# Optimization experiments

Hardware: AMD Instinct MI355X
Metric: run time of the kernel (lower is better)

The kernel has to match this reference:

```python
import jax, jax.numpy as jnp
import numpy as np

D = 4096  # domain size of every variable X, Y, Z, W


def setup_inputs() -> dict:
    key = jax.random.key(0)
    ks = jax.random.split(key, 7)
    theta0 = jax.random.normal(ks[0], (D, D), dtype=jnp.float32)  # clique (X, Y)
    theta1 = jax.random.normal(ks[1], (D, D), dtype=jnp.float32)  # clique (Y, Z)
    theta2 = jax.random.normal(ks[2], (D, D), dtype=jnp.float32)  # clique (Z, W)
    ops = {f"op{i}": jax.random.randint(ks[3 + i], (2, D), 0, D, dtype=jnp.int32)
           for i in range(4)}
    return {"theta0": theta0, "theta1": theta1, "theta2": theta2, **ops}


def _remap(proc, op, dom):
    # torch: zeros(dom).index_add_(0, op[1], proc[op[0]])
    return jnp.zeros((dom,), proc.dtype).at[op[1]].add(proc[op[0]])


def reference(theta0, theta1, theta2, op0, op1, op2, op3):
    dom = theta0.shape[0]
    # m0: clique0 -> clique1 (forward): sum over X (dim 0), remap Y, broadcast over Z
    m0 = _remap(jnp.sum(theta0, axis=0), op0, dom)
    theta1 = theta1 + m0[:, None]          # reshape_dims [True, False]
    # m1: clique1 -> clique2 (forward): sum over Y (dim 0), remap Z
    m1 = _remap(jnp.sum(theta1, axis=0), op1, dom)
    theta2 = theta2 + m1[:, None]
    # m2: clique2 -> clique1 (backward): sum over W (dim 1), subtract stored fwd msg m1
    m2 = _remap(jnp.sum(theta2, axis=1) - m1, op2, dom)
    theta1 = theta1 + m2[None, :]          # reshape_dims [False, True]
    # m3: clique1 -> clique0 (backward): sum over Z (dim 1), subtract stored fwd msg m0
    m3 = _remap(jnp.sum(theta1, axis=1) - m0, op3, dom)
    theta0 = theta0 + m3[None, :]
    return (theta0, theta1, theta2)
```

## Files before the change

kernel.cpp:

```cpp
#include <hip/hip_runtime.h>

#define D 4096

typedef float fx4 __attribute__((ext_vector_type(4)));


__global__ void __launch_bounds__(256) reduce_all_kernel(
        const float* __restrict__ t0, const float* __restrict__ t1,
        const float* __restrict__ t2, float* __restrict__ ws) {
    int b = blockIdx.x;
    if (b < 512) {
        const float* A = (b < 256) ? t0 : t1;
        float* out = ws + ((b < 256) ? 0 : D);
        int lb = b & 255;
        int c4 = (lb & 3) * 256 + threadIdx.x;
        int r0 = (lb >> 2) * 64;
        const fx4* A4 = (const fx4*)A;
        fx4 s = (fx4){0.f, 0.f, 0.f, 0.f};
        #pragma unroll 8
        for (int r = 0; r < 64; ++r) {
            s += A4[(size_t)(r0 + r) * (D / 4) + c4];
        }
        atomicAdd(&out[c4 * 4 + 0], s.x);
        atomicAdd(&out[c4 * 4 + 1], s.y);
        atomicAdd(&out[c4 * 4 + 2], s.z);
        atomicAdd(&out[c4 * 4 + 3], s.w);
    } else {
        int lb = (b - 512) & 1023;
        const float* A = (b < 1536) ? t1 : t2;
        float* out = ws + ((b < 1536) ? 2 * D : 3 * D);
        int wid = threadIdx.x >> 6, lane = threadIdx.x & 63;
        int row = lb * 4 + wid;
        const fx4* A4 = (const fx4*)(A + (size_t)row * D);
        float s = 0.f;
        #pragma unroll 4
        for (int i = lane; i < D / 4; i += 64) {
            fx4 v = A4[i];
            s += (v.x + v.y) + (v.z + v.w);
        }
        #pragma unroll
        for (int o = 32; o > 0; o >>= 1) s += __shfl_down(s, o);
        if (lane == 0) out[row] = s;
    }
}


__device__ __forceinline__ float block_sum_1024(float v, float* red) {
    #pragma unroll
    for (int o = 32; o > 0; o >>= 1) v += __shfl_down(v, o);
    int lane = threadIdx.x & 63, wid = threadIdx.x >> 6;
    if (lane == 0) red[wid] = v;
    __syncthreads();
    if (threadIdx.x == 0) {
        float t = 0.f;
        #pragma unroll
        for (int w = 0; w < 16; ++w) t += red[w];
        red[0] = t;
    }
    __syncthreads();
    float r = red[0];
    __syncthreads();
    return r;
}

__global__ void __launch_bounds__(1024) messages_kernel(
        const float* __restrict__ ws,
        const int* __restrict__ op0, const int* __restrict__ op1,
        const int* __restrict__ op2, const int* __restrict__ op3,
        float* __restrict__ ws_w) {
    const float* colsum0 = ws;
    const float* colsum1 = ws + D;
    const float* rowsum1 = ws + 2 * D;
    const float* rowsum2 = ws + 3 * D;

    __shared__ float m0[D], m1[D], m2[D], m3[D];
    __shared__ float red[16];
    int tid = threadIdx.x;

    int s0[4], d0[4], s1[4], d1[4], s2[4], d2[4], s3[4], d3[4];
    #pragma unroll
    for (int k = 0; k < 4; ++k) {
        int i = tid + k * 1024;
        s0[k] = op0[i]; d0[k] = op0[D + i];
        s1[k] = op1[i]; d1[k] = op1[D + i];
        s2[k] = op2[i]; d2[k] = op2[D + i];
        s3[k] = op3[i]; d3[k] = op3[D + i];
    }
    float g0[4], g1[4], g2[4], g3[4];
    #pragma unroll
    for (int k = 0; k < 4; ++k) {
        g0[k] = colsum0[s0[k]];
        g1[k] = colsum1[s1[k]];
        g2[k] = rowsum2[s2[k]];
        g3[k] = rowsum1[s3[k]];
    }

    #pragma unroll
    for (int k = 0; k < 4; ++k) {
        int i = tid + k * 1024;
        m0[i] = 0.f; m1[i] = 0.f; m2[i] = 0.f; m3[i] = 0.f;
    }
    __syncthreads();

    #pragma unroll
    for (int k = 0; k < 4; ++k) atomicAdd(&m0[d0[k]], g0[k]);
    __syncthreads();

    float p = 0.f;
    #pragma unroll
    for (int k = 0; k < 4; ++k) p += m0[tid + k * 1024];
    float S0 = block_sum_1024(p, red);

    #pragma unroll
    for (int k = 0; k < 4; ++k) atomicAdd(&m1[d1[k]], g1[k] + S0);
    __syncthreads();

    #pragma unroll
    for (int k = 0; k < 4; ++k)
        atomicAdd(&m2[d2[k]], g2[k] + 4095.0f * m1[s2[k]]);
    __syncthreads();

    p = 0.f;
    #pragma unroll
    for (int k = 0; k < 4; ++k) p += m2[tid + k * 1024];
    float S2 = block_sum_1024(p, red);

    #pragma unroll
    for (int k = 0; k < 4; ++k)
        atomicAdd(&m3[d3[k]], g3[k] + 4095.0f * m0[s3[k]] + S2);
    __syncthreads();

    #pragma unroll
    for (int k = 0; k < 4; ++k) {
        int i = tid + k * 1024;
        ws_w[4 * D + i] = m0[i];
        ws_w[5 * D + i] = m1[i];
        ws_w[6 * D + i] = m2[i];
        ws_w[7 * D + i] = m3[i];
    }
}

__global__ void __launch_bounds__(256) apply_kernel(
        const float* __restrict__ t0, const float* __restrict__ t1,
        const float* __restrict__ t2, const float* __restrict__ msgs,
        float* __restrict__ out) {
    int b = blockIdx.x;
    int mat = b >> 12;
    int row = b & (D - 1);
    const float* m0 = msgs + 0 * D;
    const float* m1 = msgs + 1 * D;
    const float* m2 = msgs + 2 * D;
    const float* m3 = msgs + 3 * D;
    size_t base = (size_t)row * D;
    fx4* dst = (fx4*)(out + (size_t)mat * D * D + base);

    if (mat == 0) {
        const fx4* src = (const fx4*)(t0 + base);
        const fx4* c4 = (const fx4*)m3;
        for (int i = threadIdx.x; i < D / 4; i += 256) {
            fx4 r = src[i] + c4[i];
            __builtin_nontemporal_store(r, &dst[i]);
        }
    } else if (mat == 1) {
        const fx4* src = (const fx4*)(t1 + base);
        const fx4* c4 = (const fx4*)m2;
        float rr = m0[row];
        for (int i = threadIdx.x; i < D / 4; i += 256) {
            fx4 r = src[i] + c4[i] + rr;
            __builtin_nontemporal_store(r, &dst[i]);
        }
    } else {
        const fx4* src = (const fx4*)(t2 + base);
        float rr = m1[row];
        for (int i = threadIdx.x; i < D / 4; i += 256) {
            fx4 r = src[i] + rr;
            __builtin_nontemporal_store(r, &dst[i]);
        }
    }
}

extern "C" void kernel_launch(void* const* d_in, const int* in_sizes, int n_in,
                              void* d_out, int out_size, void* d_ws, size_t ws_size,
                              hipStream_t stream) {
    const float* t0 = (const float*)d_in[0];
    const float* t1 = (const float*)d_in[1];
    const float* t2 = (const float*)d_in[2];
    const int* op0 = (const int*)d_in[3];
    const int* op1 = (const int*)d_in[4];
    const int* op2 = (const int*)d_in[5];
    const int* op3 = (const int*)d_in[6];
    float* out = (float*)d_out;
    float* ws = (float*)d_ws;

    hipMemsetAsync(ws, 0, 2 * D * sizeof(float), stream);

    reduce_all_kernel<<<2560, 256, 0, stream>>>(t0, t1, t2, ws);
    messages_kernel<<<1, 1024, 0, stream>>>(ws, op0, op1, op2, op3, ws);
    apply_kernel<<<3 * D, 256, 0, stream>>>(t0, t1, t2, ws + 4 * D, out);
}
```

Before: 143.8 us.

## Fuse theta1 row/column sums into one pass and drop atomics and memset

```diff
diff --git a/kernel.cpp b/kernel.cpp
--- a/kernel.cpp
+++ b/kernel.cpp
@@ -4,43 +4,79 @@
 
 typedef float fx4 __attribute__((ext_vector_type(4)));
 
+#define P0  0
+#define P1  262144
+#define RS1 524288
+#define RS2 528384
+#define MSG 532480
 
 __global__ void __launch_bounds__(256) reduce_all_kernel(
         const float* __restrict__ t0, const float* __restrict__ t1,
         const float* __restrict__ t2, float* __restrict__ ws) {
     int b = blockIdx.x;
-    if (b < 512) {
-        const float* A = (b < 256) ? t0 : t1;
-        float* out = ws + ((b < 256) ? 0 : D);
-        int lb = b & 255;
-        int c4 = (lb & 3) * 256 + threadIdx.x;
-        int r0 = (lb >> 2) * 64;
-        const fx4* A4 = (const fx4*)A;
-        fx4 s = (fx4){0.f, 0.f, 0.f, 0.f};
+    if (b < 256) {
+        int q = b & 3, s = b >> 2;
+        int c4 = q * 256 + threadIdx.x;
+        int r0 = s * 64;
+        const fx4* A4 = (const fx4*)t0;
+        fx4 acc = (fx4){0.f, 0.f, 0.f, 0.f};
         #pragma unroll 8
-        for (int r = 0; r < 64; ++r) {
-            s += A4[(size_t)(r0 + r) * (D / 4) + c4];
-        }
-        atomicAdd(&out[c4 * 4 + 0], s.x);
-        atomicAdd(&out[c4 * 4 + 1], s.y);
-        atomicAdd(&out[c4 * 4 + 2], s.z);
-        atomicAdd(&out[c4 * 4 + 3], s.w);
+        for (int r = 0; r < 64; ++r)
+            acc += A4[(size_t)(r0 + r) * (D / 4) + c4];
+        ((fx4*)(ws + P0))[(size_t)s * (D / 4) + c4] = acc;
+    } else if (b < 320) {
+        int s = b - 256;
+        int r0 = s * 64;
+        int wid = threadIdx.x >> 6, lane = threadIdx.x & 63;
+        const fx4* A4 = (const fx4*)t1;
+        fx4 acc[16];
+        #pragma unroll
+        for (int j = 0; j < 16; ++j) acc[j] = (fx4){0.f, 0.f, 0.f, 0.f};
+        for (int it = 0; it < 16; ++it) {
+            int row = r0 + it * 4 + wid;
+            const fx4* R = A4 + (size_t)row * (D / 4);
+            float rs = 0.f;
+            #pragma unroll
+            for (int j = 0; j < 16; ++j) {
+                fx4 v = R[lane + 64 * j];
+                acc[j] += v;
+                rs += (v.x + v.y) + (v.z + v.w);
+            }
+            #pragma unroll
+            for (int o = 32; o > 0; o >>= 1) rs += __shfl_down(rs, o);
+            if (lane == 0) ws[RS1 + row] = rs;
+        }
+        __shared__ fx4 cs[D / 4];
+        for (int ww = 0; ww < 4; ++ww) {
+            if (wid == ww) {
+                #pragma unroll
+                for (int j = 0; j < 16; ++j) {
+                    int c = lane + 64 * j;
+                    if (ww == 0) cs[c] = acc[j]; else cs[c] += acc[j];
+                }
+            }
+            __syncthreads();
+        }
+        fx4* part1 = (fx4*)(ws + P1);
+        #pragma unroll
+        for (int k = 0; k < 4; ++k) {
+            int c4 = threadIdx.x + 256 * k;
+            part1[(size_t)s * (D / 4) + c4] = cs[c4];
+        }
     } else {
-        int lb = (b - 512) & 1023;
-        const float* A = (b < 1536) ? t1 : t2;
-        float* out = ws + ((b < 1536) ? 2 * D : 3 * D);
+        int lb = b - 320;
         int wid = threadIdx.x >> 6, lane = threadIdx.x & 63;
         int row = lb * 4 + wid;
-        const fx4* A4 = (const fx4*)(A + (size_t)row * D);
-        float s = 0.f;
-        #pragma unroll 4
-        for (int i = lane; i < D / 4; i += 64) {
-            fx4 v = A4[i];
-            s += (v.x + v.y) + (v.z + v.w);
-        }
-        #pragma unroll
-        for (int o = 32; o > 0; o >>= 1) s += __shfl_down(s, o);
-        if (lane == 0) out[row] = s;
+        const fx4* R = (const fx4*)(t2 + (size_t)row * D);
+        float ssum = 0.f;
+        #pragma unroll
+        for (int j = 0; j < 16; ++j) {
+            fx4 v = R[lane + 64 * j];
+            ssum += (v.x + v.y) + (v.z + v.w);
+        }
+        #pragma unroll
+        for (int o = 32; o > 0; o >>= 1) ssum += __shfl_down(ssum, o);
+        if (lane == 0) ws[RS2 + row] = ssum;
     }
 }
 
@@ -68,11 +104,7 @@
         const int* __restrict__ op0, const int* __restrict__ op1,
         const int* __restrict__ op2, const int* __restrict__ op3,
         float* __restrict__ ws_w) {
-    const float* colsum0 = ws;
-    const float* colsum1 = ws + D;
-    const float* rowsum1 = ws + 2 * D;
-    const float* rowsum2 = ws + 3 * D;
-
+    __shared__ float cs0[D], cs1[D];
     __shared__ float m0[D], m1[D], m2[D], m3[D];
     __shared__ float red[16];
     int tid = threadIdx.x;
@@ -86,13 +118,26 @@
         s2[k] = op2[i]; d2[k] = op2[D + i];
         s3[k] = op3[i]; d3[k] = op3[D + i];
     }
-    float g0[4], g1[4], g2[4], g3[4];
-    #pragma unroll
-    for (int k = 0; k < 4; ++k) {
-        g0[k] = colsum0[s0[k]];
-        g1[k] = colsum1[s1[k]];
-        g2[k] = rowsum2[s2[k]];
-        g3[k] = rowsum1[s3[k]];
+
+    {
+        const fx4* part0 = (const fx4*)(ws + P0);
+        const fx4* part1 = (const fx4*)(ws + P1);
+        fx4 a0 = (fx4){0.f, 0.f, 0.f, 0.f};
+        fx4 a1 = (fx4){0.f, 0.f, 0.f, 0.f};
+        #pragma unroll 8
+        for (int s = 0; s < 64; ++s) {
+            a0 += part0[(size_t)s * (D / 4) + tid];
+            a1 += part1[(size_t)s * (D / 4) + tid];
+        }
+        ((fx4*)cs0)[tid] = a0;
+        ((fx4*)cs1)[tid] = a1;
+    }
+
+    float g2[4], g3[4];
+    #pragma unroll
+    for (int k = 0; k < 4; ++k) {
+        g2[k] = ws[RS2 + s2[k]];
+        g3[k] = ws[RS1 + s3[k]];
     }
 
     #pragma unroll
@@ -103,7 +148,7 @@
     __syncthreads();
 
     #pragma unroll
-    for (int k = 0; k < 4; ++k) atomicAdd(&m0[d0[k]], g0[k]);
+    for (int k = 0; k < 4; ++k) atomicAdd(&m0[d0[k]], cs0[s0[k]]);
     __syncthreads();
 
     float p = 0.f;
@@ -112,7 +157,7 @@
     float S0 = block_sum_1024(p, red);
 
     #pragma unroll
-    for (int k = 0; k < 4; ++k) atomicAdd(&m1[d1[k]], g1[k] + S0);
+    for (int k = 0; k < 4; ++k) atomicAdd(&m1[d1[k]], cs1[s1[k]] + S0);
     __syncthreads();
 
     #pragma unroll
@@ -133,10 +178,10 @@
     #pragma unroll
     for (int k = 0; k < 4; ++k) {
         int i = tid + k * 1024;
-        ws_w[4 * D + i] = m0[i];
-        ws_w[5 * D + i] = m1[i];
-        ws_w[6 * D + i] = m2[i];
-        ws_w[7 * D + i] = m3[i];
+        ws_w[MSG + 0 * D + i] = m0[i];
+        ws_w[MSG + 1 * D + i] = m1[i];
+        ws_w[MSG + 2 * D + i] = m2[i];
+        ws_w[MSG + 3 * D + i] = m3[i];
     }
 }
 
@@ -158,7 +203,7 @@
         const fx4* src = (const fx4*)(t0 + base);
         const fx4* c4 = (const fx4*)m3;
         for (int i = threadIdx.x; i < D / 4; i += 256) {
-            fx4 r = src[i] + c4[i];
+            fx4 r = __builtin_nontemporal_load(&src[i]) + c4[i];
             __builtin_nontemporal_store(r, &dst[i]);
         }
     } else if (mat == 1) {
@@ -166,14 +211,14 @@
         const fx4* c4 = (const fx4*)m2;
         float rr = m0[row];
         for (int i = threadIdx.x; i < D / 4; i += 256) {
-            fx4 r = src[i] + c4[i] + rr;
+            fx4 r = __builtin_nontemporal_load(&src[i]) + c4[i] + rr;
             __builtin_nontemporal_store(r, &dst[i]);
         }
     } else {
         const fx4* src = (const fx4*)(t2 + base);
         float rr = m1[row];
         for (int i = threadIdx.x; i < D / 4; i += 256) {
-            fx4 r = src[i] + rr;
+            fx4 r = __builtin_nontemporal_load(&src[i]) + rr;
             __builtin_nontemporal_store(r, &dst[i]);
         }
     }
@@ -192,9 +237,7 @@
     float* out = (float*)d_out;
     float* ws = (float*)d_ws;
 
-    hipMemsetAsync(ws, 0, 2 * D * sizeof(float), stream);
-
-    reduce_all_kernel<<<2560, 256, 0, stream>>>(t0, t1, t2, ws);
+    reduce_all_kernel<<<1344, 256, 0, stream>>>(t0, t1, t2, ws);
     messages_kernel<<<1, 1024, 0, stream>>>(ws, op0, op1, op2, op3, ws);
-    apply_kernel<<<3 * D, 256, 0, stream>>>(t0, t1, t2, ws + 4 * D, out);
-}
+    apply_kernel<<<3 * D, 256, 0, stream>>>(t0, t1, t2, ws + MSG, out);
+}
```

New measurement: 151.5 us. +5.4%, slower.

## Fuse theta1 row and column sums into one pass and vectorize message setup

Applied to the files above, without the earlier changes.

```diff
diff --git a/kernel.cpp b/kernel.cpp
--- a/kernel.cpp
+++ b/kernel.cpp
@@ -3,44 +3,93 @@
 #define D 4096
 
 typedef float fx4 __attribute__((ext_vector_type(4)));
-
+typedef int   ix4 __attribute__((ext_vector_type(4)));
+
+#define CS0 0
+#define CS1 D
+#define RS1 (2 * D)
+#define RS2 (3 * D)
+#define MSG (4 * D)
 
 __global__ void __launch_bounds__(256) reduce_all_kernel(
         const float* __restrict__ t0, const float* __restrict__ t1,
         const float* __restrict__ t2, float* __restrict__ ws) {
     int b = blockIdx.x;
-    if (b < 512) {
-        const float* A = (b < 256) ? t0 : t1;
-        float* out = ws + ((b < 256) ? 0 : D);
-        int lb = b & 255;
-        int c4 = (lb & 3) * 256 + threadIdx.x;
-        int r0 = (lb >> 2) * 64;
-        const fx4* A4 = (const fx4*)A;
-        fx4 s = (fx4){0.f, 0.f, 0.f, 0.f};
+    int tid = threadIdx.x;
+    if (b < 256) {
+        int q = b & 3, s = b >> 2;
+        int c4 = q * 256 + tid;
+        int r0 = s * 64;
+        const fx4* A4 = (const fx4*)t0;
+        fx4 acc = (fx4){0.f, 0.f, 0.f, 0.f};
         #pragma unroll 8
-        for (int r = 0; r < 64; ++r) {
-            s += A4[(size_t)(r0 + r) * (D / 4) + c4];
-        }
-        atomicAdd(&out[c4 * 4 + 0], s.x);
-        atomicAdd(&out[c4 * 4 + 1], s.y);
-        atomicAdd(&out[c4 * 4 + 2], s.z);
-        atomicAdd(&out[c4 * 4 + 3], s.w);
+        for (int r = 0; r < 64; ++r)
+            acc += A4[(size_t)(r0 + r) * (D / 4) + c4];
+        atomicAdd(&ws[CS0 + c4 * 4 + 0], acc.x);
+        atomicAdd(&ws[CS0 + c4 * 4 + 1], acc.y);
+        atomicAdd(&ws[CS0 + c4 * 4 + 2], acc.z);
+        atomicAdd(&ws[CS0 + c4 * 4 + 3], acc.w);
+    } else if (b < 512) {
+        int s = b - 256;
+        int r0 = s * 16;
+        const fx4* A4 = (const fx4*)t1;
+        fx4 ca0 = (fx4){0.f,0.f,0.f,0.f}, ca1 = ca0, ca2 = ca0, ca3 = ca0;
+        float rp[16];
+        #pragma unroll
+        for (int r = 0; r < 16; ++r) {
+            const fx4* R = A4 + (size_t)(r0 + r) * (D / 4);
+            fx4 v0 = R[tid];
+            fx4 v1 = R[tid + 256];
+            fx4 v2 = R[tid + 512];
+            fx4 v3 = R[tid + 768];
+            ca0 += v0; ca1 += v1; ca2 += v2; ca3 += v3;
+            fx4 t = (v0 + v1) + (v2 + v3);
+            rp[r] = (t.x + t.y) + (t.z + t.w);
+        }
+        __shared__ float rbuf[16][256];
+        #pragma unroll
+        for (int r = 0; r < 16; ++r) rbuf[r][tid] = rp[r];
+        __syncthreads();
+        int wid = tid >> 6, lane = tid & 63;
+        #pragma unroll
+        for (int k = 0; k < 4; ++k) {
+            int r = wid * 4 + k;
+            float sres = (rbuf[r][lane] + rbuf[r][lane + 64]) +
+                         (rbuf[r][lane + 128] + rbuf[r][lane + 192]);
+            #pragma unroll
+            for (int o = 32; o > 0; o >>= 1) sres += __shfl_down(sres, o);
+            if (lane == 0) ws[RS1 + r0 + r] = sres;
+        }
+        atomicAdd(&ws[CS1 + (tid        ) * 4 + 0], ca0.x);
+        atomicAdd(&ws[CS1 + (tid        ) * 4 + 1], ca0.y);
+        atomicAdd(&ws[CS1 + (tid        ) * 4 + 2], ca0.z);
+        atomicAdd(&ws[CS1 + (tid        ) * 4 + 3], ca0.w);
+        atomicAdd(&ws[CS1 + (tid +  256 ) * 4 + 0], ca1.x);
+        atomicAdd(&ws[CS1 + (tid +  256 ) * 4 + 1], ca1.y);
+        atomicAdd(&ws[CS1 + (tid +  256 ) * 4 + 2], ca1.z);
+        atomicAdd(&ws[CS1 + (tid +  256 ) * 4 + 3], ca1.w);
+        atomicAdd(&ws[CS1 + (tid +  512 ) * 4 + 0], ca2.x);
+        atomicAdd(&ws[CS1 + (tid +  512 ) * 4 + 1], ca2.y);
+        atomicAdd(&ws[CS1 + (tid +  512 ) * 4 + 2], ca2.z);
+        atomicAdd(&ws[CS1 + (tid +  512 ) * 4 + 3], ca2.w);
+        atomicAdd(&ws[CS1 + (tid +  768 ) * 4 + 0], ca3.x);
+        atomicAdd(&ws[CS1 + (tid +  768 ) * 4 + 1], ca3.y);
+        atomicAdd(&ws[CS1 + (tid +  768 ) * 4 + 2], ca3.z);
+        atomicAdd(&ws[CS1 + (tid +  768 ) * 4 + 3], ca3.w);
     } else {
-        int lb = (b - 512) & 1023;
-        const float* A = (b < 1536) ? t1 : t2;
-        float* out = ws + ((b < 1536) ? 2 * D : 3 * D);
-        int wid = threadIdx.x >> 6, lane = threadIdx.x & 63;
+        int lb = b - 512;
+        int wid = tid >> 6, lane = tid & 63;
         int row = lb * 4 + wid;
-        const fx4* A4 = (const fx4*)(A + (size_t)row * D);
-        float s = 0.f;
-        #pragma unroll 4
-        for (int i = lane; i < D / 4; i += 64) {
-            fx4 v = A4[i];
-            s += (v.x + v.y) + (v.z + v.w);
-        }
-        #pragma unroll
-        for (int o = 32; o > 0; o >>= 1) s += __shfl_down(s, o);
-        if (lane == 0) out[row] = s;
+        const fx4* R = (const fx4*)(t2 + (size_t)row * D);
+        float ssum = 0.f;
+        #pragma unroll
+        for (int j = 0; j < 16; ++j) {
+            fx4 v = R[lane + 64 * j];
+            ssum += (v.x + v.y) + (v.z + v.w);
+        }
+        #pragma unroll
+        for (int o = 32; o > 0; o >>= 1) ssum += __shfl_down(ssum, o);
+        if (lane == 0) ws[RS2 + row] = ssum;
     }
 }
 
@@ -68,48 +117,35 @@
         const int* __restrict__ op0, const int* __restrict__ op1,
         const int* __restrict__ op2, const int* __restrict__ op3,
         float* __restrict__ ws_w) {
-    const float* colsum0 = ws;
-    const float* colsum1 = ws + D;
-    const float* rowsum1 = ws + 2 * D;
-    const float* rowsum2 = ws + 3 * D;
-
     __shared__ float m0[D], m1[D], m2[D], m3[D];
     __shared__ float red[16];
     int tid = threadIdx.x;
 
-    int s0[4], d0[4], s1[4], d1[4], s2[4], d2[4], s3[4], d3[4];
+    ix4 s0 = ((const ix4*)op0)[tid], d0 = ((const ix4*)op0)[1024 + tid];
+    ix4 s1 = ((const ix4*)op1)[tid], d1 = ((const ix4*)op1)[1024 + tid];
+    ix4 s2 = ((const ix4*)op2)[tid], d2 = ((const ix4*)op2)[1024 + tid];
+    ix4 s3 = ((const ix4*)op3)[tid], d3 = ((const ix4*)op3)[1024 + tid];
+
+    float g0[4], g1[4], g2[4], g3[4];
     #pragma unroll
     for (int k = 0; k < 4; ++k) {
-        int i = tid + k * 1024;
-        s0[k] = op0[i]; d0[k] = op0[D + i];
-        s1[k] = op1[i]; d1[k] = op1[D + i];
-        s2[k] = op2[i]; d2[k] = op2[D + i];
-        s3[k] = op3[i]; d3[k] = op3[D + i];
-    }
-    float g0[4], g1[4], g2[4], g3[4];
-    #pragma unroll
-    for (int k = 0; k < 4; ++k) {
-        g0[k] = colsum0[s0[k]];
-        g1[k] = colsum1[s1[k]];
-        g2[k] = rowsum2[s2[k]];
-        g3[k] = rowsum1[s3[k]];
-    }
-
-    #pragma unroll
-    for (int k = 0; k < 4; ++k) {
-        int i = tid + k * 1024;
-        m0[i] = 0.f; m1[i] = 0.f; m2[i] = 0.f; m3[i] = 0.f;
-    }
+        g0[k] = ws[CS0 + s0[k]];
+        g1[k] = ws[CS1 + s1[k]];
+        g2[k] = ws[RS2 + s2[k]];
+        g3[k] = ws[RS1 + s3[k]];
+    }
+
+    fx4 z = (fx4){0.f, 0.f, 0.f, 0.f};
+    ((fx4*)m0)[tid] = z; ((fx4*)m1)[tid] = z;
+    ((fx4*)m2)[tid] = z; ((fx4*)m3)[tid] = z;
     __syncthreads();
 
     #pragma unroll
     for (int k = 0; k < 4; ++k) atomicAdd(&m0[d0[k]], g0[k]);
     __syncthreads();
 
-    float p = 0.f;
-    #pragma unroll
-    for (int k = 0; k < 4; ++k) p += m0[tid + k * 1024];
-    float S0 = block_sum_1024(p, red);
+    fx4 pv = ((fx4*)m0)[tid];
+    float S0 = block_sum_1024((pv.x + pv.y) + (pv.z + pv.w), red);
 
     #pragma unroll
     for (int k = 0; k < 4; ++k) atomicAdd(&m1[d1[k]], g1[k] + S0);
@@ -120,24 +156,18 @@
         atomicAdd(&m2[d2[k]], g2[k] + 4095.0f * m1[s2[k]]);
     __syncthreads();
 
-    p = 0.f;
-    #pragma unroll
-    for (int k = 0; k < 4; ++k) p += m2[tid + k * 1024];
-    float S2 = block_sum_1024(p, red);
+    pv = ((fx4*)m2)[tid];
+    float S2 = block_sum_1024((pv.x + pv.y) + (pv.z + pv.w), red);
 
     #pragma unroll
     for (int k = 0; k < 4; ++k)
         atomicAdd(&m3[d3[k]], g3[k] + 4095.0f * m0[s3[k]] + S2);
     __syncthreads();
 
-    #pragma unroll
-    for (int k = 0; k < 4; ++k) {
-        int i = tid + k * 1024;
-        ws_w[4 * D + i] = m0[i];
-        ws_w[5 * D + i] = m1[i];
-        ws_w[6 * D + i] = m2[i];
-        ws_w[7 * D + i] = m3[i];
-    }
+    ((fx4*)(ws_w + MSG + 0 * D))[tid] = ((fx4*)m0)[tid];
+    ((fx4*)(ws_w + MSG + 1 * D))[tid] = ((fx4*)m1)[tid];
+    ((fx4*)(ws_w + MSG + 2 * D))[tid] = ((fx4*)m2)[tid];
+    ((fx4*)(ws_w + MSG + 3 * D))[tid] = ((fx4*)m3)[tid];
 }
 
 __global__ void __launch_bounds__(256) apply_kernel(
@@ -158,7 +188,7 @@
         const fx4* src = (const fx4*)(t0 + base);
         const fx4* c4 = (const fx4*)m3;
         for (int i = threadIdx.x; i < D / 4; i += 256) {
-            fx4 r = src[i] + c4[i];
+            fx4 r = __builtin_nontemporal_load(&src[i]) + c4[i];
             __builtin_nontemporal_store(r, &dst[i]);
         }
     } else if (mat == 1) {
@@ -166,14 +196,14 @@
         const fx4* c4 = (const fx4*)m2;
         float rr = m0[row];
         for (int i = threadIdx.x; i < D / 4; i += 256) {
-            fx4 r = src[i] + c4[i] + rr;
+            fx4 r = __builtin_nontemporal_load(&src[i]) + c4[i] + rr;
             __builtin_nontemporal_store(r, &dst[i]);
         }
     } else {
         const fx4* src = (const fx4*)(t2 + base);
         float rr = m1[row];
         for (int i = threadIdx.x; i < D / 4; i += 256) {
-            fx4 r = src[i] + rr;
+            fx4 r = __builtin_nontemporal_load(&src[i]) + rr;
             __builtin_nontemporal_store(r, &dst[i]);
         }
     }
@@ -194,7 +224,7 @@
 
     hipMemsetAsync(ws, 0, 2 * D * sizeof(float), stream);
 
-    reduce_all_kernel<<<2560, 256, 0, stream>>>(t0, t1, t2, ws);
+    reduce_all_kernel<<<1536, 256, 0, stream>>>(t0, t1, t2, ws);
     messages_kernel<<<1, 1024, 0, stream>>>(ws, op0, op1, op2, op3, ws);
-    apply_kernel<<<3 * D, 256, 0, stream>>>(t0, t1, t2, ws + 4 * D, out);
-}
+    apply_kernel<<<3 * D, 256, 0, stream>>>(t0, t1, t2, ws + MSG, out);
+}
```

Measured after the change: 171.8 us. 1.19x slower.
